# Optimization experiments

Hardware: AMD Instinct MI355X
Metric: run time of the kernel (lower is better)

## Reference

```python
import jax, jax.numpy as jnp
import numpy as np

B, NQ, NK = 2, 1024, 1024
QD, KVD, OD = 1024, 1024, 1024
H, DH = 8, 64
INNER = H * DH  # 512
FF_INNER = 4 * OD


def _ln(x, w, b, eps=1e-5):
    m = jnp.mean(x, axis=-1, keepdims=True)
    v = jnp.mean((x - m) ** 2, axis=-1, keepdims=True)
    return (x - m) / jnp.sqrt(v + eps) * w + b


def _attn(q, k, v, h):
    # q:[b,nq,h*d] k,v:[b,nk,h*d] -> [b,nq,h*d]
    b, nq, _ = q.shape
    nk = k.shape[1]
    qh = q.reshape(b, nq, h, -1).transpose(0, 2, 1, 3)
    kh = k.reshape(b, nk, h, -1).transpose(0, 2, 1, 3)
    vh = v.reshape(b, nk, h, -1).transpose(0, 2, 1, 3)
    scale = qh.shape[-1] ** -0.5
    sim = jnp.einsum('bhid,bhjd->bhij', qh * scale, kh)
    a = jax.nn.softmax(sim, axis=-1)
    o = jnp.einsum('bhij,bhjd->bhid', a, vh)
    return o.transpose(0, 2, 1, 3).reshape(b, nq, -1)


def setup_inputs() -> dict:
    key = jax.random.key(0)
    ks = jax.random.split(key, 16)
    w = lambda k, shp: jax.random.normal(k, shp, dtype=jnp.float32) * 0.02
    return {
        'query_feats': jax.random.normal(ks[0], (B, NQ, QD), dtype=jnp.float32),
        'kv_feats_wt': jax.random.normal(ks[1], (B, NK, KVD), dtype=jnp.float32),
        'nq_w': jnp.ones((QD,), jnp.float32), 'nq_b': jnp.zeros((QD,), jnp.float32),
        'nkv_w': jnp.ones((KVD,), jnp.float32), 'nkv_b': jnp.zeros((KVD,), jnp.float32),
        'wq_cross': w(ks[2], (INNER, QD)),
        'wkv_cross': w(ks[3], (2 * INNER, KVD)),
        'wqkv_self': w(ks[4], (3 * INNER, QD)),
        'gn_w': jnp.ones((INNER,), jnp.float32), 'gn_b': jnp.zeros((INNER,), jnp.float32),
        'mha_in_w': w(ks[5], (3 * INNER, INNER)),
        'mha_out_w': w(ks[6], (INNER, INNER)),
        'mix_w': w(ks[7], (2, INNER)), 'mix_b': jnp.zeros((2,), jnp.float32),
        'w_out': w(ks[8], (OD, INNER)),
        'ff_ln_w': jnp.ones((OD,), jnp.float32), 'ff_ln_b': jnp.zeros((OD,), jnp.float32),
        'ff_fc1': w(ks[9], (FF_INNER, OD)),
        'ff_fc2': w(ks[10], (OD, FF_INNER)),
        'ff_gate': jnp.ones((1,), jnp.float32),
    }


def reference(query_feats, kv_feats_wt, nq_w, nq_b, nkv_w, nkv_b, wq_cross,
              wkv_cross, wqkv_self, gn_w, gn_b, mha_in_w, mha_out_w, mix_w,
              mix_b, w_out, ff_ln_w, ff_ln_b, ff_fc1, ff_fc2, ff_gate):
    # mode == 'full'
    kvn = _ln(kv_feats_wt, nkv_w, nkv_b)

    # wt self-attention branch
    qkv_wt = kvn @ wqkv_self.T
    q_wt, k_wt, v_wt = jnp.split(qkv_wt, 3, axis=-1)
    wt_out = _attn(q_wt, k_wt, v_wt, H) @ w_out.T

    qn = _ln(query_feats, nq_w, nq_b)

    # cross attention
    q_c = qn @ wq_cross.T
    k_c, v_c = jnp.split(kvn @ wkv_cross.T, 2, axis=-1)
    cross_out = _attn(q_c, k_c, v_c, H)

    # self attention on query
    q_s, k_s, v_s = jnp.split(qn @ wqkv_self.T, 3, axis=-1)
    self_out = _attn(q_s, k_s, v_s, H)

    # gating MHA (shared gate_norm)
    son = _ln(self_out, gn_w, gn_b)
    con = _ln(cross_out, gn_w, gn_b)
    wq_g, wk_g, wv_g = jnp.split(mha_in_w, 3, axis=0)
    gate_ctx = _attn(son @ wq_g.T, con @ wk_g.T, con @ wv_g.T, H) @ mha_out_w.T

    mix = jax.nn.softmax(gate_ctx @ mix_w.T + mix_b, axis=-1)
    mixed = mix[..., 0:1] * self_out + mix[..., 1:2] * cross_out
    delta = mixed @ w_out.T

    # FeedForward with gate
    y = _ln(delta, ff_ln_w, ff_ln_b)
    y = jax.nn.gelu(y @ ff_fc1.T, approximate=False) @ ff_fc2.T
    delta = delta + ff_gate * y

    return jnp.stack([delta, wt_out])  # [2, B, NQ, OD]
```

## Files before the change

### kernel.cpp

```cpp
#include <hip/hip_runtime.h>
#include <math.h>


#define M_ROWS 2048
#define SEQ    1024

typedef unsigned short u16;
typedef __attribute__((ext_vector_type(8))) short short8;
typedef __attribute__((ext_vector_type(4))) float f32x4;

__device__ inline u16 f2b(float f) {
    unsigned u = __builtin_bit_cast(unsigned, f);
    u += 0x7FFFu + ((u >> 16) & 1u);
    return (u16)(u >> 16);
}
__device__ inline float b2f(u16 h) {
    return __builtin_bit_cast(float, (unsigned)h << 16);
}

__device__ inline void gload16(const u16* g, u16* l) {
    __builtin_amdgcn_global_load_lds(
        (const __attribute__((address_space(1))) void*)g,
        (__attribute__((address_space(3))) void*)l, 16, 0, 0);
}

__device__ __forceinline__ int aswz(int prow, int chunk) {
    return prow * 32 + ((chunk ^ ((prow >> 1) & 3)) << 3);
}

struct CvtPack { const float* s[8]; u16* d[8]; };

__global__ __launch_bounds__(256)
void cvt8_kernel(CvtPack p)
{
    constexpr int pre[9] = {0, 1536, 2048, 3072, 3840, 4096, 4608, 8704, 12800};
    const int b = blockIdx.x;
    int seg = 0;
    #pragma unroll
    for (int i = 1; i < 8; ++i) seg += (b >= pre[i]);
    const int off = (b - pre[seg]) * 1024 + threadIdx.x * 4;
    const float4 v = *reinterpret_cast<const float4*>(p.s[seg] + off);
    ushort4 o;
    o.x = f2b(v.x); o.y = f2b(v.y); o.z = f2b(v.z); o.w = f2b(v.w);
    *reinterpret_cast<ushort4*>(p.d[seg] + off) = o;
}

__global__ __launch_bounds__(256)
void ln_dual(const float* __restrict__ x0, const float* __restrict__ w0,
             const float* __restrict__ b0, u16* __restrict__ out0,
             const float* __restrict__ x1, const float* __restrict__ w1,
             const float* __restrict__ b1, u16* __restrict__ out1, int D)
{
    const int r = blockIdx.x;
    const int sel = r >= M_ROWS;
    const size_t row = sel ? r - M_ROWS : r;
    const float* x = sel ? x1 : x0;
    const float* w = sel ? w1 : w0;
    const float* bias = sel ? b1 : b0;
    u16* out = sel ? out1 : out0;
    const float* xr = x + row * (size_t)D;
    const int c = threadIdx.x * 4;
    float4 v = make_float4(0.f, 0.f, 0.f, 0.f);
    if (c < D) v = *reinterpret_cast<const float4*>(&xr[c]);
    float sum = v.x + v.y + v.z + v.w;
    float sq  = v.x*v.x + v.y*v.y + v.z*v.z + v.w*v.w;
    #pragma unroll
    for (int off = 32; off > 0; off >>= 1) {
        sum += __shfl_down(sum, off);
        sq  += __shfl_down(sq,  off);
    }
    __shared__ float s1[4], s2[4];
    const int wid = threadIdx.x >> 6;
    if ((threadIdx.x & 63) == 0) { s1[wid] = sum; s2[wid] = sq; }
    __syncthreads();
    const float tsum = s1[0] + s1[1] + s1[2] + s1[3];
    const float tsq  = s2[0] + s2[1] + s2[2] + s2[3];
    const float mean = tsum / (float)D;
    const float var  = tsq / (float)D - mean * mean;
    const float rstd = rsqrtf(var + 1e-5f);
    if (c < D) {
        ushort4 o;
        o.x = f2b((v.x - mean) * rstd * w[c+0] + bias[c+0]);
        o.y = f2b((v.y - mean) * rstd * w[c+1] + bias[c+1]);
        o.z = f2b((v.z - mean) * rstd * w[c+2] + bias[c+2]);
        o.w = f2b((v.w - mean) * rstd * w[c+3] + bias[c+3]);
        *reinterpret_cast<ushort4*>(&out[row * (size_t)D + c]) = o;
    }
}

__global__ __launch_bounds__(256)
void ln_bf16(const float* __restrict__ x, const float* __restrict__ w,
             const float* __restrict__ bias, u16* __restrict__ out, int D)
{
    const size_t row = blockIdx.x;
    const float* xr = x + row * (size_t)D;
    const int c = threadIdx.x * 4;
    float4 v = make_float4(0.f, 0.f, 0.f, 0.f);
    if (c < D) v = *reinterpret_cast<const float4*>(&xr[c]);
    float sum = v.x + v.y + v.z + v.w;
    float sq  = v.x*v.x + v.y*v.y + v.z*v.z + v.w*v.w;
    #pragma unroll
    for (int off = 32; off > 0; off >>= 1) {
        sum += __shfl_down(sum, off);
        sq  += __shfl_down(sq,  off);
    }
    __shared__ float s1[4], s2[4];
    const int wid = threadIdx.x >> 6;
    if ((threadIdx.x & 63) == 0) { s1[wid] = sum; s2[wid] = sq; }
    __syncthreads();
    const float tsum = s1[0] + s1[1] + s1[2] + s1[3];
    const float tsq  = s2[0] + s2[1] + s2[2] + s2[3];
    const float mean = tsum / (float)D;
    const float var  = tsq / (float)D - mean * mean;
    const float rstd = rsqrtf(var + 1e-5f);
    if (c < D) {
        ushort4 o;
        o.x = f2b((v.x - mean) * rstd * w[c+0] + bias[c+0]);
        o.y = f2b((v.y - mean) * rstd * w[c+1] + bias[c+1]);
        o.z = f2b((v.z - mean) * rstd * w[c+2] + bias[c+2]);
        o.w = f2b((v.w - mean) * rstd * w[c+3] + bias[c+3]);
        *reinterpret_cast<ushort4*>(&out[row * (size_t)D + c]) = o;
    }
}

__device__ __forceinline__ void gemm64_core(
    const u16* __restrict__ A, const u16* __restrict__ W, u16* __restrict__ C,
    int N, int K, int m0, int n0, u16* As, u16* Ws)
{
    constexpr int PF = 3, LPT = 2, RD = 4;
    const int tid  = threadIdx.x;
    const int lane = tid & 63;
    const int wave = tid >> 6;
    const int wr = wave >> 1, wc = wave & 1;

    const int srow = tid >> 2;
    const int scol = (((tid & 3) ^ ((srow >> 1) & 3))) * 8;
    const u16* Ag = A + (size_t)(m0 + srow) * K + scol;
    const u16* Wg = W + (size_t)(n0 + srow) * K + scol;

    const int fr = lane & 15;
    const int fq = lane >> 4;

    f32x4 acc[2][2] = {};

    auto stage = [&](int buf, int k0) {
        gload16(Ag + k0, &As[buf * 2048 + tid * 8]);
        gload16(Wg + k0, &Ws[buf * 2048 + tid * 8]);
    };
    auto compute = [&](int buf) {
        short8 a[2], b[2];
        #pragma unroll
        for (int m = 0; m < 2; ++m) {
            const int r = wr * 32 + m * 16 + fr;
            a[m] = *reinterpret_cast<const short8*>(&As[buf * 2048 + aswz(r, fq)]);
        }
        #pragma unroll
        for (int n = 0; n < 2; ++n) {
            const int r = wc * 32 + n * 16 + fr;
            b[n] = *reinterpret_cast<const short8*>(&Ws[buf * 2048 + aswz(r, fq)]);
        }
        #pragma unroll
        for (int m = 0; m < 2; ++m)
            #pragma unroll
            for (int n = 0; n < 2; ++n)
                acc[m][n] = __builtin_amdgcn_mfma_f32_16x16x32_bf16(
                    a[m], b[n], acc[m][n], 0, 0, 0);
    };

    const int nt = K / 32;
    #pragma unroll
    for (int i = 0; i < PF; ++i) stage(i, i * 32);

    int cbuf = 0, sbuf = PF;
    for (int t = 0; t <= nt - PF; ++t) {
        asm volatile("s_waitcnt vmcnt(%0)\n\ts_barrier"
                     :: "n"((PF - 1) * LPT) : "memory");
        if (t + PF < nt) {
            stage(sbuf, (t + PF) * 32);
            if (++sbuf == RD) sbuf = 0;
        }
        compute(cbuf);
        if (++cbuf == RD) cbuf = 0;
    }
    #pragma unroll
    for (int i = 1; i < PF; ++i) {
        asm volatile("s_waitcnt vmcnt(%0)\n\ts_barrier"
                     :: "n"((PF - 1 - i) * LPT) : "memory");
        compute(cbuf);
        if (++cbuf == RD) cbuf = 0;
    }

    #pragma unroll
    for (int m = 0; m < 2; ++m)
        #pragma unroll
        for (int j = 0; j < 4; ++j) {
            const size_t row = (size_t)(m0 + wr * 32 + m * 16 + fq * 4 + j);
            #pragma unroll
            for (int n = 0; n < 2; ++n)
                C[row * (size_t)N + (size_t)(n0 + wc * 32 + n * 16 + fr)] =
                    f2b(acc[m][n][j]);
        }
}

template<int BM, int BN, int EPI, int OB>
__global__ __launch_bounds__(256)
void gemm_mfma(const u16* __restrict__ A, const u16* __restrict__ W,
               void* __restrict__ Cv, int N, int K,
               const float* __restrict__ gatep, int kchunk)
{
    constexpr int MF  = BM / 32;
    constexpr int NF  = BN / 32;
    constexpr int LPT = BM / 64 + BN / 64;
    constexpr int PF  = 3;
    constexpr int RD  = 4;
    __shared__ __align__(16) u16 As[RD][BM * 32];
    __shared__ __align__(16) u16 Ws[RD][BN * 32];
    const int tid  = threadIdx.x;
    const int lane = tid & 63;
    const int wave = tid >> 6;
    const int wr = wave >> 1, wc = wave & 1;

    const int nwg = gridDim.x * gridDim.y;
    const int bid = blockIdx.y * gridDim.x + blockIdx.x;
    const int nid = (bid & 7) * (nwg >> 3) + (bid >> 3);
    const int by  = nid % gridDim.y;
    const int bx  = nid / gridDim.y;
    const int m0 = by * BM, n0 = bx * BN;
    const int kz = blockIdx.z * kchunk;

    const int srow = tid >> 2;
    const int scol = (((tid & 3) ^ ((srow >> 1) & 3))) * 8;
    const u16* Ag = A + (size_t)(m0 + srow) * K + scol + kz;
    const u16* Wg = W + (size_t)(n0 + srow) * K + scol + kz;

    const int fr = lane & 15;
    const int fq = lane >> 4;

    f32x4 acc[MF][NF] = {};

    auto stage = [&](int buf, int k0) {
        #pragma unroll
        for (int i = 0; i < BM / 64; ++i)
            gload16(Ag + k0 + (size_t)(i * 64) * K, &As[buf][tid * 8 + i * 2048]);
        #pragma unroll
        for (int i = 0; i < BN / 64; ++i)
            gload16(Wg + k0 + (size_t)(i * 64) * K, &Ws[buf][tid * 8 + i * 2048]);
    };
    auto compute = [&](int buf) {
        short8 a[MF], b[NF];
        #pragma unroll
        for (int m = 0; m < MF; ++m) {
            const int r = wr * (BM / 2) + m * 16 + fr;
            a[m] = *reinterpret_cast<const short8*>(&As[buf][aswz(r, fq)]);
        }
        #pragma unroll
        for (int n = 0; n < NF; ++n) {
            const int r = wc * (BN / 2) + n * 16 + fr;
            b[n] = *reinterpret_cast<const short8*>(&Ws[buf][aswz(r, fq)]);
        }
        #pragma unroll
        for (int m = 0; m < MF; ++m)
            #pragma unroll
            for (int n = 0; n < NF; ++n)
                acc[m][n] = __builtin_amdgcn_mfma_f32_16x16x32_bf16(
                    a[m], b[n], acc[m][n], 0, 0, 0);
    };

    const int nt = kchunk / 32;
    #pragma unroll
    for (int i = 0; i < PF; ++i) stage(i, i * 32);

    int cbuf = 0, sbuf = PF;
    for (int t = 0; t <= nt - PF; ++t) {
        asm volatile("s_waitcnt vmcnt(%0)\n\ts_barrier"
                     :: "n"((PF - 1) * LPT) : "memory");
        if (t + PF < nt) {
            stage(sbuf, (t + PF) * 32);
            if (++sbuf == RD) sbuf = 0;
        }
        compute(cbuf);
        if (++cbuf == RD) cbuf = 0;
    }
    #pragma unroll
    for (int i = 1; i < PF; ++i) {
        asm volatile("s_waitcnt vmcnt(%0)\n\ts_barrier"
                     :: "n"((PF - 1 - i) * LPT) : "memory");
        compute(cbuf);
        if (++cbuf == RD) cbuf = 0;
    }

    float* Cz = (float*)Cv + (size_t)blockIdx.z * M_ROWS * N;
    const float gate = (EPI == 2) ? gatep[0] : 0.f;
    #pragma unroll
    for (int m = 0; m < MF; ++m) {
        #pragma unroll
        for (int j = 0; j < 4; ++j) {
            const size_t row = (size_t)(m0 + wr * (BM / 2) + m * 16 + fq * 4 + j);
            #pragma unroll
            for (int n = 0; n < NF; ++n) {
                float v = acc[m][n][j];
                const size_t idx = row * (size_t)N + (size_t)(n0 + wc * (BN / 2) + n * 16 + fr);
                if (EPI == 1) v = 0.5f * v * (1.f + erff(v * 0.70710678118654752f));
                if (OB) {
                    ((u16*)Cv)[idx] = f2b(v);
                } else {
                    if (EPI == 2) Cz[idx] = Cz[idx] + gate * v;
                    else          Cz[idx] = v;
                }
            }
        }
    }
}

struct GemmPack4 { const u16* A[4]; const u16* W[4]; u16* C[4]; int N[4]; };

__global__ __launch_bounds__(256)
void gemm_bat4(GemmPack4 p)
{
    __shared__ __align__(16) u16 As[4][2048];
    __shared__ __align__(16) u16 Ws[4][2048];
    constexpr int pre[5] = {0, 768, 1024, 1536, 2304};
    const int nwg = gridDim.x * gridDim.y;
    const int bid = blockIdx.y * gridDim.x + blockIdx.x;
    const int nid = (bid & 7) * (nwg >> 3) + (bid >> 3);
    int seg = 0;
    #pragma unroll
    for (int i = 1; i < 4; ++i) seg += (nid >= pre[i]);
    const int idx = nid - pre[seg];
    const int nx  = p.N[seg] >> 6;
    const int bx  = idx % nx;
    const int by  = idx / nx;
    gemm64_core(p.A[seg], p.W[seg], p.C[seg], p.N[seg], 1024,
                by * 64, bx * 64, &As[0][0], &Ws[0][0]);
}

struct GemmPack3 { const u16* A[3]; const u16* W[3]; u16* C[3]; };

__global__ __launch_bounds__(256)
void gemm_bat3(GemmPack3 p)
{
    __shared__ __align__(16) u16 As[4][2048];
    __shared__ __align__(16) u16 Ws[4][2048];
    const int nwg = gridDim.x * gridDim.y;
    const int bid = blockIdx.y * gridDim.x + blockIdx.x;
    const int nid = (bid & 7) * (nwg >> 3) + (bid >> 3);
    const int z = nid % 3;
    const int r = nid / 3;
    const int bx = r & 7;
    const int by = r >> 3;
    gemm64_core(p.A[z], p.W[z], p.C[z], 512, 512,
                by * 64, bx * 64, &As[0][0], &Ws[0][0]);
}

__global__ __launch_bounds__(256)
void redk(const float* __restrict__ p, const float* __restrict__ gatep,
          float* __restrict__ C)
{
    const int i = (blockIdx.x * 256 + threadIdx.x) * 4;
    const float g = gatep[0];
    const float4 a = *reinterpret_cast<const float4*>(p + i);
    const float4 b = *reinterpret_cast<const float4*>(p + 2097152 + i);
    const float4 c = *reinterpret_cast<const float4*>(p + 4194304 + i);
    const float4 d = *reinterpret_cast<const float4*>(p + 6291456 + i);
    float4 o = *reinterpret_cast<float4*>(C + i);
    o.x += g * ((a.x + b.x) + (c.x + d.x));
    o.y += g * ((a.y + b.y) + (c.y + d.y));
    o.z += g * ((a.z + b.z) + (c.z + d.z));
    o.w += g * ((a.w + b.w) + (c.w + d.w));
    *reinterpret_cast<float4*>(C + i) = o;
}

struct AttnPack {
    const u16* Q[3]; const u16* K[3]; const u16* V[3]; void* O[3];
    int qs[3], ks[3], vs[3], os[3], ob[3];
};

__global__ __launch_bounds__(256)
void attn_mfma(AttnPack p, int NP)
{
    const int nwg = gridDim.x * gridDim.y;
    const int bid = blockIdx.y * gridDim.x + blockIdx.x;
    const int nid = (bid & 7) * (nwg >> 3) + (bid >> 3);
    const int z  = nid % NP;
    const int r_ = nid / NP;
    const int qt = r_ & 15;
    const int bh = r_ >> 4;

    const u16* __restrict__ Q = p.Q[z];
    const u16* __restrict__ K = p.K[z];
    const u16* __restrict__ V = p.V[z];
    void* __restrict__ Ov = p.O[z];
    const int qs = p.qs[z], ks = p.ks[z], vs = p.vs[z], os = p.os[z];
    const int ob = p.ob[z];

    __shared__ __align__(16) u16 Ks[2][128 * 32];
    __shared__ __align__(16) u16 Vt[2][128 * 32];
    __shared__ __align__(16) u16 Ps[4][32 * 32];
    const int tid  = threadIdx.x;
    const int lane = tid & 63;
    const int wave = tid >> 6;
    const int fr = lane & 15;
    const int fq = lane >> 4;

    const int b   = bh >> 3;
    const int hc  = (bh & 7) * 64;
    const size_t qrow0 = (size_t)b * SEQ + (size_t)qt * 64;
    const size_t krow0 = (size_t)b * SEQ;

    short8 qf[2];
    {
        const u16* qp = Q + (qrow0 + wave * 16 + fr) * qs + hc + fq * 8;
        qf[0] = *reinterpret_cast<const short8*>(qp);
        qf[1] = *reinterpret_cast<const short8*>(qp + 32);
    }

    const int skr = tid >> 2;
    const int skc = (tid & 3) * 16;
    const int svk = (tid >> 4) * 4;
    const int svd = (tid & 15) * 4;

    const int kprow = (skc >= 32 ? 64 : 0) + skr;
    const int kc0   = (skc & 31) >> 3;
    const int vbase  = (svk >= 32) ? 64 : 0;
    const int vchunk = (svk & 31) >> 3;
    const int vpos   = svk & 7;

    short8 kreg0, kreg1;
    ushort4 vr0, vr1, vr2, vr3;
    auto load_tile = [&](int kt) {
        const u16* kp = K + (krow0 + kt * 64 + skr) * ks + hc + skc;
        kreg0 = *reinterpret_cast<const short8*>(kp);
        kreg1 = *reinterpret_cast<const short8*>(kp + 8);
        const u16* vp = V + (krow0 + kt * 64 + svk) * vs + hc + svd;
        vr0 = *reinterpret_cast<const ushort4*>(vp);
        vr1 = *reinterpret_cast<const ushort4*>(vp + vs);
        vr2 = *reinterpret_cast<const ushort4*>(vp + 2 * (size_t)vs);
        vr3 = *reinterpret_cast<const ushort4*>(vp + 3 * (size_t)vs);
    };
    auto write_tile = [&](int bf) {
        *reinterpret_cast<short8*>(&Ks[bf][aswz(kprow, kc0)])     = kreg0;
        *reinterpret_cast<short8*>(&Ks[bf][aswz(kprow, kc0 + 1)]) = kreg1;
        uint2 w;
        #pragma unroll
        for (int i = 0; i < 4; ++i) {
            u16* dst = &Vt[bf][aswz(vbase + svd + i, vchunk) + vpos];
            unsigned lo, hi;
            if (i == 0) { lo = (unsigned)vr0.x | ((unsigned)vr1.x << 16);
                          hi = (unsigned)vr2.x | ((unsigned)vr3.x << 16); }
            else if (i == 1) { lo = (unsigned)vr0.y | ((unsigned)vr1.y << 16);
                               hi = (unsigned)vr2.y | ((unsigned)vr3.y << 16); }
            else if (i == 2) { lo = (unsigned)vr0.z | ((unsigned)vr1.z << 16);
                               hi = (unsigned)vr2.z | ((unsigned)vr3.z << 16); }
            else { lo = (unsigned)vr0.w | ((unsigned)vr1.w << 16);
                   hi = (unsigned)vr2.w | ((unsigned)vr3.w << 16); }
            w.x = lo; w.y = hi;
            *reinterpret_cast<uint2*>(dst) = w;
        }
    };

    float m_run = -1e30f, l_run = 0.f;
    f32x4 acc[4] = {};

    load_tile(0);
    write_tile(0);
    __syncthreads();

    constexpr int NT = SEQ / 64;
    for (int kt = 0; kt < NT; ++kt) {
        const int bf = kt & 1;
        if (kt + 1 < NT) load_tile(kt + 1);

        f32x4 st[4] = {};
        #pragma unroll
        for (int kn = 0; kn < 4; ++kn) {
            const int r = kn * 16 + fr;
            const short8 ka0 = *reinterpret_cast<const short8*>(
                &Ks[bf][aswz(r, fq)]);
            const short8 ka1 = *reinterpret_cast<const short8*>(
                &Ks[bf][aswz(64 + r, fq)]);
            st[kn] = __builtin_amdgcn_mfma_f32_16x16x32_bf16(ka0, qf[0], st[kn], 0, 0, 0);
            st[kn] = __builtin_amdgcn_mfma_f32_16x16x32_bf16(ka1, qf[1], st[kn], 0, 0, 0);
        }

        float mx = -1e30f;
        #pragma unroll
        for (int kn = 0; kn < 4; ++kn)
            #pragma unroll
            for (int r = 0; r < 4; ++r) {
                st[kn][r] *= 0.125f;
                mx = fmaxf(mx, st[kn][r]);
            }
        mx = fmaxf(mx, __shfl_xor(mx, 16, 64));
        mx = fmaxf(mx, __shfl_xor(mx, 32, 64));
        const float mnew = fmaxf(m_run, mx);
        const float corr = __expf(m_run - mnew);
        m_run = mnew;
        float psum = 0.f;
        #pragma unroll
        for (int kn = 0; kn < 4; ++kn) {
            const float p0 = __expf(st[kn][0] - mnew);
            const float p1 = __expf(st[kn][1] - mnew);
            const float p2 = __expf(st[kn][2] - mnew);
            const float p3 = __expf(st[kn][3] - mnew);
            psum += (p0 + p1) + (p2 + p3);
            uint2 w;
            w.x = (unsigned)f2b(p0) | ((unsigned)f2b(p1) << 16);
            w.y = (unsigned)f2b(p2) | ((unsigned)f2b(p3) << 16);
            const int prow = (kn >> 1) * 16 + fr;
            const int pcol = (kn & 1) * 16 + fq * 4;
            *reinterpret_cast<uint2*>(
                &Ps[wave][aswz(prow, pcol >> 3) + (pcol & 7)]) = w;
        }
        psum += __shfl_xor(psum, 16, 64);
        psum += __shfl_xor(psum, 32, 64);
        l_run = l_run * corr + psum;

        float cq[4];
        #pragma unroll
        for (int j = 0; j < 4; ++j) cq[j] = __shfl(corr, fq * 4 + j, 64);
        #pragma unroll
        for (int nd = 0; nd < 4; ++nd)
            #pragma unroll
            for (int j = 0; j < 4; ++j)
                acc[nd][j] *= cq[j];

        short8 pa0 = *reinterpret_cast<const short8*>(&Ps[wave][aswz(fr, fq)]);
        short8 pa1 = *reinterpret_cast<const short8*>(&Ps[wave][aswz(16 + fr, fq)]);
        #pragma unroll
        for (int nd = 0; nd < 4; ++nd) {
            const int d = nd * 16 + fr;
            const short8 vb0 = *reinterpret_cast<const short8*>(
                &Vt[bf][aswz(d, fq)]);
            const short8 vb1 = *reinterpret_cast<const short8*>(
                &Vt[bf][aswz(64 + d, fq)]);
            acc[nd] = __builtin_amdgcn_mfma_f32_16x16x32_bf16(pa0, vb0, acc[nd], 0, 0, 0);
            acc[nd] = __builtin_amdgcn_mfma_f32_16x16x32_bf16(pa1, vb1, acc[nd], 0, 0, 0);
        }

        if (kt + 1 < NT) write_tile(bf ^ 1);
        __syncthreads();
    }

    float iq[4];
    #pragma unroll
    for (int j = 0; j < 4; ++j) iq[j] = 1.f / __shfl(l_run, fq * 4 + j, 64);
    #pragma unroll
    for (int j = 0; j < 4; ++j) {
        const size_t orow = (qrow0 + wave * 16 + fq * 4 + j) * os + hc;
        #pragma unroll
        for (int nd = 0; nd < 4; ++nd) {
            const float v = acc[nd][j] * iq[j];
            if (ob) ((u16*)Ov)[orow + nd * 16 + fr] = f2b(v);
            else    ((float*)Ov)[orow + nd * 16 + fr] = v;
        }
    }
}

__global__ __launch_bounds__(256)
void mix_kernel(const float* __restrict__ gctx, const float* __restrict__ mixw,
                const float* __restrict__ mixb, const float* __restrict__ so,
                const float* __restrict__ co, u16* __restrict__ mixed)
{
    const size_t row = blockIdx.x;
    const float* g = gctx + row * 512;
    float d0 = 0.f, d1 = 0.f;
    for (int c = threadIdx.x; c < 512; c += 256) {
        const float gv = g[c];
        d0 = fmaf(gv, mixw[c], d0);
        d1 = fmaf(gv, mixw[512 + c], d1);
    }
    #pragma unroll
    for (int off = 32; off > 0; off >>= 1) {
        d0 += __shfl_down(d0, off);
        d1 += __shfl_down(d1, off);
    }
    __shared__ float sA[4], sB[4];
    const int wid = threadIdx.x >> 6;
    if ((threadIdx.x & 63) == 0) { sA[wid] = d0; sB[wid] = d1; }
    __syncthreads();
    const float t0 = sA[0] + sA[1] + sA[2] + sA[3] + mixb[0];
    const float t1 = sB[0] + sB[1] + sB[2] + sB[3] + mixb[1];
    const float mx = fmaxf(t0, t1);
    const float e0 = __expf(t0 - mx), e1 = __expf(t1 - mx);
    const float inv = 1.f / (e0 + e1);
    const float w0 = e0 * inv, w1 = e1 * inv;
    for (int c = threadIdx.x; c < 512; c += 256)
        mixed[row * 512 + c] = f2b(w0 * so[row * 512 + c] + w1 * co[row * 512 + c]);
}

extern "C" void kernel_launch(void* const* d_in, const int* in_sizes, int n_in,
                              void* d_out, int out_size, void* d_ws, size_t ws_size,
                              hipStream_t stream)
{
    const float* query     = (const float*)d_in[0];
    const float* kvwt      = (const float*)d_in[1];
    const float* nq_w      = (const float*)d_in[2];
    const float* nq_b      = (const float*)d_in[3];
    const float* nkv_w     = (const float*)d_in[4];
    const float* nkv_b     = (const float*)d_in[5];
    const float* wq_cross  = (const float*)d_in[6];
    const float* wkv_cross = (const float*)d_in[7];
    const float* wqkv_self = (const float*)d_in[8];
    const float* gn_w      = (const float*)d_in[9];
    const float* gn_b      = (const float*)d_in[10];
    const float* mha_in_w  = (const float*)d_in[11];
    const float* mha_out_w = (const float*)d_in[12];
    const float* mix_w     = (const float*)d_in[13];
    const float* mix_b     = (const float*)d_in[14];
    const float* w_out     = (const float*)d_in[15];
    const float* ff_ln_w   = (const float*)d_in[16];
    const float* ff_ln_b   = (const float*)d_in[17];
    const float* ff_fc1    = (const float*)d_in[18];
    const float* ff_fc2    = (const float*)d_in[19];
    const float* ff_gate   = (const float*)d_in[20];

    float* delta_out = (float*)d_out;
    float* wt_out    = (float*)d_out + (size_t)M_ROWS * 1024;

    char* wsb = (char*)d_ws;
    u16*   qkv_b   = (u16*)  (wsb + 0);
    u16*   kv_c_b  = (u16*)  (wsb + 6291456);
    u16*   q_c_b   = (u16*)  (wsb + 10485760);
    float* cross_f = (float*)(wsb + 12582912);
    float* self_f  = (float*)(wsb + 16777216);
    u16*   kvn_b   = (u16*)  (wsb + 20971520);
    u16*   qn_b    = (u16*)  (wsb + 25165824);
    u16*   wta_b   = (u16*)  (wsb + 29360128);
    u16*   con_b   = (u16*)  (wsb + 31457280);
    u16*   gq_b    = qkv_b;
    u16*   gk_b    = qkv_b + 1048576;
    u16*   gv_b    = qkv_b + 2097152;
    float* gctx_f  = (float*)kv_c_b;
    u16*   gattn_b = kvn_b;
    u16*   mixed_b = kvn_b + 1048576;
    u16*   lnd_b   = qn_b;
    u16*   son_b   = wta_b;
    u16*   ffh_b   = qkv_b;
    float* part_f  = (float*)(wsb + 16777216);
    u16*   qkv_s_b = (u16*)  (wsb + 59768832);
    u16* wqkv_self_b = (u16*)(wsb + 33554432);
    u16* wq_cross_b  = (u16*)(wsb + 36700160);
    u16* wkv_cross_b = (u16*)(wsb + 37748736);
    u16* mha_in_b    = (u16*)(wsb + 39845888);
    u16* mha_out_b   = (u16*)(wsb + 41418752);
    u16* w_out_b     = (u16*)(wsb + 41943040);
    u16* ff_fc1_b    = (u16*)(wsb + 42991616);
    u16* ff_fc2_b    = (u16*)(wsb + 51380224);

    const dim3 blk(256);

    CvtPack cp;
    cp.s[0] = wqkv_self; cp.d[0] = wqkv_self_b;
    cp.s[1] = wq_cross;  cp.d[1] = wq_cross_b;
    cp.s[2] = wkv_cross; cp.d[2] = wkv_cross_b;
    cp.s[3] = mha_in_w;  cp.d[3] = mha_in_b;
    cp.s[4] = mha_out_w; cp.d[4] = mha_out_b;
    cp.s[5] = w_out;     cp.d[5] = w_out_b;
    cp.s[6] = ff_fc1;    cp.d[6] = ff_fc1_b;
    cp.s[7] = ff_fc2;    cp.d[7] = ff_fc2_b;
    cvt8_kernel<<<dim3(12800), blk, 0, stream>>>(cp);

    ln_dual<<<dim3(2 * M_ROWS), blk, 0, stream>>>(
        kvwt, nkv_w, nkv_b, kvn_b, query, nq_w, nq_b, qn_b, 1024);

    GemmPack4 g4;
    g4.A[0] = kvn_b; g4.W[0] = wqkv_self_b; g4.C[0] = qkv_b;   g4.N[0] = 1536;
    g4.A[1] = qn_b;  g4.W[1] = wq_cross_b;  g4.C[1] = q_c_b;   g4.N[1] = 512;
    g4.A[2] = kvn_b; g4.W[2] = wkv_cross_b; g4.C[2] = kv_c_b;  g4.N[2] = 1024;
    g4.A[3] = qn_b;  g4.W[3] = wqkv_self_b; g4.C[3] = qkv_s_b; g4.N[3] = 1536;
    gemm_bat4<<<dim3(72, 32), blk, 0, stream>>>(g4);

    AttnPack ap;
    ap.Q[0] = qkv_b;    ap.K[0] = qkv_b + 512;    ap.V[0] = qkv_b + 1024;    ap.O[0] = wta_b;
    ap.qs[0] = 1536; ap.ks[0] = 1536; ap.vs[0] = 1536; ap.os[0] = 512; ap.ob[0] = 1;
    ap.Q[1] = q_c_b;    ap.K[1] = kv_c_b;         ap.V[1] = kv_c_b + 512;    ap.O[1] = cross_f;
    ap.qs[1] = 512;  ap.ks[1] = 1024; ap.vs[1] = 1024; ap.os[1] = 512; ap.ob[1] = 0;
    ap.Q[2] = qkv_s_b;  ap.K[2] = qkv_s_b + 512;  ap.V[2] = qkv_s_b + 1024;  ap.O[2] = self_f;
    ap.qs[2] = 1536; ap.ks[2] = 1536; ap.vs[2] = 1536; ap.os[2] = 512; ap.ob[2] = 0;
    attn_mfma<<<dim3(48, 16), blk, 0, stream>>>(ap, 3);

    gemm_mfma<64,128,0,0><<<dim3(8, 32), blk, 0, stream>>>(wta_b, w_out_b, wt_out, 1024, 512, nullptr, 512);
    ln_dual<<<dim3(2 * M_ROWS), blk, 0, stream>>>(
        self_f, gn_w, gn_b, son_b, cross_f, gn_w, gn_b, con_b, 512);
    GemmPack3 g3;
    g3.A[0] = son_b; g3.W[0] = mha_in_b;            g3.C[0] = gq_b;
    g3.A[1] = con_b; g3.W[1] = mha_in_b + 512*512;  g3.C[1] = gk_b;
    g3.A[2] = con_b; g3.W[2] = mha_in_b + 1024*512; g3.C[2] = gv_b;
    gemm_bat3<<<dim3(24, 32), blk, 0, stream>>>(g3);
    AttnPack gp;
    gp.Q[0] = gq_b; gp.K[0] = gk_b; gp.V[0] = gv_b; gp.O[0] = gattn_b;
    gp.qs[0] = 512; gp.ks[0] = 512; gp.vs[0] = 512; gp.os[0] = 512; gp.ob[0] = 1;
    gp.Q[1] = gp.Q[0]; gp.K[1] = gp.K[0]; gp.V[1] = gp.V[0]; gp.O[1] = gp.O[0];
    gp.qs[1] = 512; gp.ks[1] = 512; gp.vs[1] = 512; gp.os[1] = 512; gp.ob[1] = 1;
    gp.Q[2] = gp.Q[0]; gp.K[2] = gp.K[0]; gp.V[2] = gp.V[0]; gp.O[2] = gp.O[0];
    gp.qs[2] = 512; gp.ks[2] = 512; gp.vs[2] = 512; gp.os[2] = 512; gp.ob[2] = 1;
    attn_mfma<<<dim3(16, 16), blk, 0, stream>>>(gp, 1);
    gemm_mfma<64,64,0,0><<<dim3(8, 32), blk, 0, stream>>>(gattn_b, mha_out_b, gctx_f, 512, 512, nullptr, 512);
    mix_kernel<<<dim3(M_ROWS), blk, 0, stream>>>(gctx_f, mix_w, mix_b, self_f, cross_f, mixed_b);
    gemm_mfma<64,128,0,0><<<dim3(8, 32), blk, 0, stream>>>(mixed_b, w_out_b, delta_out, 1024, 512, nullptr, 512);
    ln_bf16<<<dim3(M_ROWS), blk, 0, stream>>>(delta_out, ff_ln_w, ff_ln_b, lnd_b, 1024);
    gemm_mfma<64,64,1,1><<<dim3(64, 32), blk, 0, stream>>>(lnd_b, ff_fc1_b, ffh_b, 4096, 1024, nullptr, 1024);
    gemm_mfma<64,64,0,0><<<dim3(16, 32, 4), blk, 0, stream>>>(ffh_b, ff_fc2_b, part_f, 1024, 4096, nullptr, 1024);
    redk<<<dim3(2048), blk, 0, stream>>>(part_f, ff_gate, delta_out);
}
```

Before: 277.1 us.

## Use 128x64 tiles for projection and FFN GEMMs, batch wt-out with gate projections

Adds a 128x64 GEMM core and uses it for the batched initial QKV projections, halving the block count and increasing A-tile reuse. The FFN fc1/fc2 GEMMs also switch to 128-row tiles. The wt_out projection is merged into the gate Q/K/V batched launch, which requires moving son_b to a fresh workspace region, and the delta GEMM goes to 64x64 tiles. The goal is fewer launches and better reuse, at the cost of more LDS per block and fewer blocks, which may reduce occupancy.

```diff
diff --git a/kernel.cpp b/kernel.cpp
--- a/kernel.cpp
+++ b/kernel.cpp
@@ -124,8 +124,8 @@
 }
 
 __device__ __forceinline__ void gemm64_core(
-    const u16* __restrict__ A, const u16* __restrict__ W, u16* __restrict__ C,
-    int N, int K, int m0, int n0, u16* As, u16* Ws)
+    const u16* __restrict__ A, const u16* __restrict__ W, void* __restrict__ C,
+    int ob, int N, int K, int m0, int n0, u16* As, u16* Ws)
 {
     constexpr int PF = 3, LPT = 2, RD = 4;
     const int tid  = threadIdx.x;
@@ -195,6 +195,88 @@
         #pragma unroll
         for (int j = 0; j < 4; ++j) {
             const size_t row = (size_t)(m0 + wr * 32 + m * 16 + fq * 4 + j);
+            #pragma unroll
+            for (int n = 0; n < 2; ++n) {
+                const size_t idx = row * (size_t)N + (size_t)(n0 + wc * 32 + n * 16 + fr);
+                if (ob) ((u16*)C)[idx]  = f2b(acc[m][n][j]);
+                else    ((float*)C)[idx] = acc[m][n][j];
+            }
+        }
+}
+
+__device__ __forceinline__ void gemm128_core(
+    const u16* __restrict__ A, const u16* __restrict__ W, u16* __restrict__ C,
+    int N, int K, int m0, int n0, u16* As, u16* Ws)
+{
+    constexpr int PF = 3, LPT = 3, RD = 4;
+    const int tid  = threadIdx.x;
+    const int lane = tid & 63;
+    const int wave = tid >> 6;
+    const int wr = wave >> 1, wc = wave & 1;
+
+    const int srow = tid >> 2;
+    const int scol = (((tid & 3) ^ ((srow >> 1) & 3))) * 8;
+    const u16* Ag = A + (size_t)(m0 + srow) * K + scol;
+    const u16* Wg = W + (size_t)(n0 + srow) * K + scol;
+
+    const int fr = lane & 15;
+    const int fq = lane >> 4;
+
+    f32x4 acc[4][2] = {};
+
+    auto stage = [&](int buf, int k0) {
+        gload16(Ag + k0,                  &As[buf * 4096 + tid * 8]);
+        gload16(Ag + k0 + (size_t)64 * K, &As[buf * 4096 + tid * 8 + 2048]);
+        gload16(Wg + k0,                  &Ws[buf * 2048 + tid * 8]);
+    };
+    auto compute = [&](int buf) {
+        short8 a[4], b[2];
+        #pragma unroll
+        for (int m = 0; m < 4; ++m) {
+            const int r = wr * 64 + m * 16 + fr;
+            a[m] = *reinterpret_cast<const short8*>(&As[buf * 4096 + aswz(r, fq)]);
+        }
+        #pragma unroll
+        for (int n = 0; n < 2; ++n) {
+            const int r = wc * 32 + n * 16 + fr;
+            b[n] = *reinterpret_cast<const short8*>(&Ws[buf * 2048 + aswz(r, fq)]);
+        }
+        #pragma unroll
+        for (int m = 0; m < 4; ++m)
+            #pragma unroll
+            for (int n = 0; n < 2; ++n)
+                acc[m][n] = __builtin_amdgcn_mfma_f32_16x16x32_bf16(
+                    a[m], b[n], acc[m][n], 0, 0, 0);
+    };
+
+    const int nt = K / 32;
+    #pragma unroll
+    for (int i = 0; i < PF; ++i) stage(i, i * 32);
+
+    int cbuf = 0, sbuf = PF;
+    for (int t = 0; t <= nt - PF; ++t) {
+        asm volatile("s_waitcnt vmcnt(%0)\n\ts_barrier"
+                     :: "n"((PF - 1) * LPT) : "memory");
+        if (t + PF < nt) {
+            stage(sbuf, (t + PF) * 32);
+            if (++sbuf == RD) sbuf = 0;
+        }
+        compute(cbuf);
+        if (++cbuf == RD) cbuf = 0;
+    }
+    #pragma unroll
+    for (int i = 1; i < PF; ++i) {
+        asm volatile("s_waitcnt vmcnt(%0)\n\ts_barrier"
+                     :: "n"((PF - 1 - i) * LPT) : "memory");
+        compute(cbuf);
+        if (++cbuf == RD) cbuf = 0;
+    }
+
+    #pragma unroll
+    for (int m = 0; m < 4; ++m)
+        #pragma unroll
+        for (int j = 0; j < 4; ++j) {
+            const size_t row = (size_t)(m0 + wr * 64 + m * 16 + fq * 4 + j);
             #pragma unroll
             for (int n = 0; n < 2; ++n)
                 C[row * (size_t)N + (size_t)(n0 + wc * 32 + n * 16 + fr)] =
@@ -317,9 +399,9 @@
 __global__ __launch_bounds__(256)
 void gemm_bat4(GemmPack4 p)
 {
-    __shared__ __align__(16) u16 As[4][2048];
+    __shared__ __align__(16) u16 As[4][4096];
     __shared__ __align__(16) u16 Ws[4][2048];
-    constexpr int pre[5] = {0, 768, 1024, 1536, 2304};
+    constexpr int pre[5] = {0, 384, 512, 768, 1152};
     const int nwg = gridDim.x * gridDim.y;
     const int bid = blockIdx.y * gridDim.x + blockIdx.x;
     const int nid = (bid & 7) * (nwg >> 3) + (bid >> 3);
@@ -330,25 +412,29 @@
     const int nx  = p.N[seg] >> 6;
     const int bx  = idx % nx;
     const int by  = idx / nx;
-    gemm64_core(p.A[seg], p.W[seg], p.C[seg], p.N[seg], 1024,
-                by * 64, bx * 64, &As[0][0], &Ws[0][0]);
-}
-
-struct GemmPack3 { const u16* A[3]; const u16* W[3]; u16* C[3]; };
-
-__global__ __launch_bounds__(256)
-void gemm_bat3(GemmPack3 p)
+    gemm128_core(p.A[seg], p.W[seg], p.C[seg], p.N[seg], 1024,
+                 by * 128, bx * 64, &As[0][0], &Ws[0][0]);
+}
+
+struct GemmPack4b { const u16* A[4]; const u16* W[4]; void* C[4]; int N[4]; int ob[4]; };
+
+__global__ __launch_bounds__(256)
+void gemm_bat4b(GemmPack4b p)
 {
     __shared__ __align__(16) u16 As[4][2048];
     __shared__ __align__(16) u16 Ws[4][2048];
+    constexpr int pre[5] = {0, 512, 768, 1024, 1280};
     const int nwg = gridDim.x * gridDim.y;
     const int bid = blockIdx.y * gridDim.x + blockIdx.x;
     const int nid = (bid & 7) * (nwg >> 3) + (bid >> 3);
-    const int z = nid % 3;
-    const int r = nid / 3;
-    const int bx = r & 7;
-    const int by = r >> 3;
-    gemm64_core(p.A[z], p.W[z], p.C[z], 512, 512,
+    int seg = 0;
+    #pragma unroll
+    for (int i = 1; i < 4; ++i) seg += (nid >= pre[i]);
+    const int idx = nid - pre[seg];
+    const int nx  = p.N[seg] >> 6;
+    const int bx  = idx % nx;
+    const int by  = idx / nx;
+    gemm64_core(p.A[seg], p.W[seg], p.C[seg], p.ob[seg], p.N[seg], 512,
                 by * 64, bx * 64, &As[0][0], &Ws[0][0]);
 }
 
@@ -634,10 +720,10 @@
     u16*   gattn_b = kvn_b;
     u16*   mixed_b = kvn_b + 1048576;
     u16*   lnd_b   = qn_b;
-    u16*   son_b   = wta_b;
     u16*   ffh_b   = qkv_b;
     float* part_f  = (float*)(wsb + 16777216);
     u16*   qkv_s_b = (u16*)  (wsb + 59768832);
+    u16*   son_b   = (u16*)  (wsb + 66060288);
     u16* wqkv_self_b = (u16*)(wsb + 33554432);
     u16* wq_cross_b  = (u16*)(wsb + 36700160);
     u16* wkv_cross_b = (u16*)(wsb + 37748736);
@@ -668,7 +754,7 @@
     g4.A[1] = qn_b;  g4.W[1] = wq_cross_b;  g4.C[1] = q_c_b;   g4.N[1] = 512;
     g4.A[2] = kvn_b; g4.W[2] = wkv_cross_b; g4.C[2] = kv_c_b;  g4.N[2] = 1024;
     g4.A[3] = qn_b;  g4.W[3] = wqkv_self_b; g4.C[3] = qkv_s_b; g4.N[3] = 1536;
-    gemm_bat4<<<dim3(72, 32), blk, 0, stream>>>(g4);
+    gemm_bat4<<<dim3(36, 32), blk, 0, stream>>>(g4);
 
     AttnPack ap;
     ap.Q[0] = qkv_b;    ap.K[0] = qkv_b + 512;    ap.V[0] = qkv_b + 1024;    ap.O[0] = wta_b;
@@ -679,14 +765,16 @@
     ap.qs[2] = 1536; ap.ks[2] = 1536; ap.vs[2] = 1536; ap.os[2] = 512; ap.ob[2] = 0;
     attn_mfma<<<dim3(48, 16), blk, 0, stream>>>(ap, 3);
 
-    gemm_mfma<64,128,0,0><<<dim3(8, 32), blk, 0, stream>>>(wta_b, w_out_b, wt_out, 1024, 512, nullptr, 512);
     ln_dual<<<dim3(2 * M_ROWS), blk, 0, stream>>>(
         self_f, gn_w, gn_b, son_b, cross_f, gn_w, gn_b, con_b, 512);
-    GemmPack3 g3;
-    g3.A[0] = son_b; g3.W[0] = mha_in_b;            g3.C[0] = gq_b;
-    g3.A[1] = con_b; g3.W[1] = mha_in_b + 512*512;  g3.C[1] = gk_b;
-    g3.A[2] = con_b; g3.W[2] = mha_in_b + 1024*512; g3.C[2] = gv_b;
-    gemm_bat3<<<dim3(24, 32), blk, 0, stream>>>(g3);
+
+    GemmPack4b g4b;
+    g4b.A[0] = wta_b; g4b.W[0] = w_out_b;             g4b.C[0] = wt_out; g4b.N[0] = 1024; g4b.ob[0] = 0;
+    g4b.A[1] = son_b; g4b.W[1] = mha_in_b;            g4b.C[1] = gq_b;   g4b.N[1] = 512;  g4b.ob[1] = 1;
+    g4b.A[2] = con_b; g4b.W[2] = mha_in_b + 512*512;  g4b.C[2] = gk_b;   g4b.N[2] = 512;  g4b.ob[2] = 1;
+    g4b.A[3] = con_b; g4b.W[3] = mha_in_b + 1024*512; g4b.C[3] = gv_b;   g4b.N[3] = 512;  g4b.ob[3] = 1;
+    gemm_bat4b<<<dim3(40, 32), blk, 0, stream>>>(g4b);
+
     AttnPack gp;
     gp.Q[0] = gq_b; gp.K[0] = gk_b; gp.V[0] = gv_b; gp.O[0] = gattn_b;
     gp.qs[0] = 512; gp.ks[0] = 512; gp.vs[0] = 512; gp.os[0] = 512; gp.ob[0] = 1;
@@ -697,9 +785,9 @@
     attn_mfma<<<dim3(16, 16), blk, 0, stream>>>(gp, 1);
     gemm_mfma<64,64,0,0><<<dim3(8, 32), blk, 0, stream>>>(gattn_b, mha_out_b, gctx_f, 512, 512, nullptr, 512);
     mix_kernel<<<dim3(M_ROWS), blk, 0, stream>>>(gctx_f, mix_w, mix_b, self_f, cross_f, mixed_b);
-    gemm_mfma<64,128,0,0><<<dim3(8, 32), blk, 0, stream>>>(mixed_b, w_out_b, delta_out, 1024, 512, nullptr, 512);
+    gemm_mfma<64,64,0,0><<<dim3(16, 32), blk, 0, stream>>>(mixed_b, w_out_b, delta_out, 1024, 512, nullptr, 512);
     ln_bf16<<<dim3(M_ROWS), blk, 0, stream>>>(delta_out, ff_ln_w, ff_ln_b, lnd_b, 1024);
-    gemm_mfma<64,64,1,1><<<dim3(64, 32), blk, 0, stream>>>(lnd_b, ff_fc1_b, ffh_b, 4096, 1024, nullptr, 1024);
-    gemm_mfma<64,64,0,0><<<dim3(16, 32, 4), blk, 0, stream>>>(ffh_b, ff_fc2_b, part_f, 1024, 4096, nullptr, 1024);
+    gemm_mfma<128,64,1,1><<<dim3(64, 16), blk, 0, stream>>>(lnd_b, ff_fc1_b, ffh_b, 4096, 1024, nullptr, 1024);
+    gemm_mfma<128,64,0,0><<<dim3(16, 16, 4), blk, 0, stream>>>(ffh_b, ff_fc2_b, part_f, 1024, 4096, nullptr, 1024);
     redk<<<dim3(2048), blk, 0, stream>>>(part_f, ff_gate, delta_out);
 }
```

Result: faster. 262.6 us (-5.2%).
